# Kernel tuning notes

Hardware: AMD Instinct MI355X
Metric: run time of the kernel (lower is better)

Reference implementation:

```python
import jax, jax.numpy as jnp
import numpy as np

SPIKE_PROB = 0.3


def setup_inputs() -> dict:
    key = jax.random.key(0)
    T, B, C, H, W = 4, 32, 128, 56, 56
    u = jax.random.uniform(key, (T, B, C, H, W), dtype=jnp.float32)
    spikes = (u < SPIKE_PROB).astype(jnp.float32)  # binary spike trains
    return {"spikes": spikes, "TIME": T}


def reference(spikes, TIME):
    # spikes: [TIME, B, C, H, W] binary spike tensor, one slice per forward call.
    # Replicates Sparsity_Checker over a full TIME window:
    #   spike_collector accumulates spikes over t;
    #   sparsity_ratio = mean over t of per-step zero fraction (divided by TIME at t==TIME);
    #   temp_sparsity_ratio_of_collector = zero fraction of final collector;
    #   unique(return_counts) on integer-valued collector == bincount over 0..TIME.
    total = spikes[0].size  # elements per timestep

    # per-step zero fractions, then average over TIME (matches /= self.TIME)
    per_step_zero = jnp.sum(spikes == 0, axis=tuple(range(1, spikes.ndim)))  # [TIME]
    sparsity_ratio = jnp.sum(per_step_zero.astype(jnp.float32)) / (total * TIME)

    # final accumulated collector (state after the last forward call)
    collector = jnp.sum(spikes, axis=0)  # [B, C, H, W], integer-valued 0..TIME

    coll_zero_frac = jnp.sum(collector == 0).astype(jnp.float32) / total

    # histogram of collector values: unique_vals are 0..TIME, counts via bincount
    unique_counts = jnp.bincount(collector.astype(jnp.int32).ravel(), length=TIME + 1)

    # module returns the input spike unchanged; stats are side outputs
    return spikes, sparsity_ratio, coll_zero_frac, unique_counts
```

## Files before the change

### kernel.cpp

```cpp
#include <hip/hip_runtime.h>


constexpr int T_STEPS = 4;

__global__ __launch_bounds__(256) void spike_stats_kernel(
    const float4* __restrict__ in, float4* __restrict__ out,
    unsigned int* __restrict__ hist, int nvec)
{
    __shared__ unsigned int lhist[5];
    if (threadIdx.x < 5) lhist[threadIdx.x] = 0u;
    __syncthreads();

    unsigned long long packed = 0ull;

    const int stride = gridDim.x * blockDim.x;
    for (int v = blockIdx.x * blockDim.x + threadIdx.x; v < nvec; v += stride) {
        float4 a0 = in[0 * nvec + v];
        float4 a1 = in[1 * nvec + v];
        float4 a2 = in[2 * nvec + v];
        float4 a3 = in[3 * nvec + v];
        out[0 * nvec + v] = a0;
        out[1 * nvec + v] = a1;
        out[2 * nvec + v] = a2;
        out[3 * nvec + v] = a3;
        int cx = (int)(a0.x + a1.x + a2.x + a3.x);
        int cy = (int)(a0.y + a1.y + a2.y + a3.y);
        int cz = (int)(a0.z + a1.z + a2.z + a3.z);
        int cw = (int)(a0.w + a1.w + a2.w + a3.w);
        packed += (1ull << (cx * 12)) + (1ull << (cy * 12))
                + (1ull << (cz * 12)) + (1ull << (cw * 12));
    }

#pragma unroll
    for (int off = 32; off > 0; off >>= 1)
        packed += __shfl_down(packed, off, 64);

    if ((threadIdx.x & 63) == 0) {
#pragma unroll
        for (int k = 0; k < 5; ++k)
            atomicAdd(&lhist[k], (unsigned int)((packed >> (12 * k)) & 0xFFFull));
    }
    __syncthreads();

    if (threadIdx.x < 5)
        atomicAdd(&hist[threadIdx.x], lhist[threadIdx.x]);
}

__global__ void finalize_kernel(const unsigned int* __restrict__ hist,
                                float* __restrict__ tail, double total)
{
    if (threadIdx.x == 0 && blockIdx.x == 0) {
        double spikes_sum = 0.0;
#pragma unroll
        for (int k = 0; k < 5; ++k)
            spikes_sum += (double)k * (double)hist[k];
        double denom = total * (double)T_STEPS;
        tail[0] = (float)((denom - spikes_sum) / denom);
        tail[1] = (float)((double)hist[0] / total);
#pragma unroll
        for (int k = 0; k < 5; ++k)
            tail[2 + k] = (float)hist[k];
    }
}

extern "C" void kernel_launch(void* const* d_in, const int* in_sizes, int n_in,
                              void* d_out, int out_size, void* d_ws, size_t ws_size,
                              hipStream_t stream)
{
    const float* spikes = (const float*)d_in[0];
    float* out = (float*)d_out;

    const long n = (long)in_sizes[0];
    const long per_t = n / T_STEPS;
    const int nvec = (int)(per_t / 4);

    unsigned int* hist = (unsigned int*)d_ws;
    hipMemsetAsync(d_ws, 0, 5 * sizeof(unsigned int), stream);

    spike_stats_kernel<<<dim3(1024), dim3(256), 0, stream>>>(
        (const float4*)spikes, (float4*)out, hist, nvec);

    finalize_kernel<<<dim3(1), dim3(64), 0, stream>>>(hist, out + n, (double)per_t);
}
```

Before: 348.9 us.

## Fuse finalize into main kernel, use nontemporal loads/stores, double grid size

Switches global loads and stores to nontemporal builtins so the streamed copy does not pollute caches. It folds the separate finalize kernel into the stats kernel using a last-block-done counter, which removes one launch. It also doubles the grid from 1024 to 2048 blocks and vectorizes the four-way sum. The last-block pattern adds a threadfence and one more atomic per block.

New measurement: 443.6 us. 1.27x slower.

```diff
diff --git a/kernel.cpp b/kernel.cpp
--- a/kernel.cpp
+++ b/kernel.cpp
@@ -3,11 +3,15 @@
 
 constexpr int T_STEPS = 4;
 
+typedef float vfloat4 __attribute__((ext_vector_type(4)));
+
 __global__ __launch_bounds__(256) void spike_stats_kernel(
-    const float4* __restrict__ in, float4* __restrict__ out,
-    unsigned int* __restrict__ hist, int nvec)
+    const vfloat4* __restrict__ in, vfloat4* __restrict__ out,
+    unsigned int* __restrict__ hist,
+    float* __restrict__ tail, int nvec, double total)
 {
     __shared__ unsigned int lhist[5];
+    __shared__ unsigned int s_prev;
     if (threadIdx.x < 5) lhist[threadIdx.x] = 0u;
     __syncthreads();
 
@@ -15,20 +19,17 @@
 
     const int stride = gridDim.x * blockDim.x;
     for (int v = blockIdx.x * blockDim.x + threadIdx.x; v < nvec; v += stride) {
-        float4 a0 = in[0 * nvec + v];
-        float4 a1 = in[1 * nvec + v];
-        float4 a2 = in[2 * nvec + v];
-        float4 a3 = in[3 * nvec + v];
-        out[0 * nvec + v] = a0;
-        out[1 * nvec + v] = a1;
-        out[2 * nvec + v] = a2;
-        out[3 * nvec + v] = a3;
-        int cx = (int)(a0.x + a1.x + a2.x + a3.x);
-        int cy = (int)(a0.y + a1.y + a2.y + a3.y);
-        int cz = (int)(a0.z + a1.z + a2.z + a3.z);
-        int cw = (int)(a0.w + a1.w + a2.w + a3.w);
-        packed += (1ull << (cx * 12)) + (1ull << (cy * 12))
-                + (1ull << (cz * 12)) + (1ull << (cw * 12));
+        vfloat4 a0 = __builtin_nontemporal_load(&in[0 * nvec + v]);
+        vfloat4 a1 = __builtin_nontemporal_load(&in[1 * nvec + v]);
+        vfloat4 a2 = __builtin_nontemporal_load(&in[2 * nvec + v]);
+        vfloat4 a3 = __builtin_nontemporal_load(&in[3 * nvec + v]);
+        __builtin_nontemporal_store(a0, &out[0 * nvec + v]);
+        __builtin_nontemporal_store(a1, &out[1 * nvec + v]);
+        __builtin_nontemporal_store(a2, &out[2 * nvec + v]);
+        __builtin_nontemporal_store(a3, &out[3 * nvec + v]);
+        vfloat4 s = a0 + a1 + a2 + a3;
+        packed += (1ull << ((int)s.x * 12)) + (1ull << ((int)s.y * 12))
+                + (1ull << ((int)s.z * 12)) + (1ull << ((int)s.w * 12));
     }
 
 #pragma unroll
@@ -44,22 +45,28 @@
 
     if (threadIdx.x < 5)
         atomicAdd(&hist[threadIdx.x], lhist[threadIdx.x]);
-}
+    __syncthreads();
 
-__global__ void finalize_kernel(const unsigned int* __restrict__ hist,
-                                float* __restrict__ tail, double total)
-{
-    if (threadIdx.x == 0 && blockIdx.x == 0) {
+    if (threadIdx.x == 0) {
+        __threadfence();
+        s_prev = atomicAdd(&hist[5], 1u);
+    }
+    __syncthreads();
+    if (threadIdx.x == 0 && s_prev == gridDim.x - 1) {
+        unsigned int h[5];
+#pragma unroll
+        for (int k = 0; k < 5; ++k)
+            h[k] = atomicAdd(&hist[k], 0u);
         double spikes_sum = 0.0;
 #pragma unroll
         for (int k = 0; k < 5; ++k)
-            spikes_sum += (double)k * (double)hist[k];
+            spikes_sum += (double)k * (double)h[k];
         double denom = total * (double)T_STEPS;
         tail[0] = (float)((denom - spikes_sum) / denom);
-        tail[1] = (float)((double)hist[0] / total);
+        tail[1] = (float)((double)h[0] / total);
 #pragma unroll
         for (int k = 0; k < 5; ++k)
-            tail[2 + k] = (float)hist[k];
+            tail[2 + k] = (float)h[k];
     }
 }
 
@@ -75,10 +82,8 @@
     const int nvec = (int)(per_t / 4);
 
     unsigned int* hist = (unsigned int*)d_ws;
-    hipMemsetAsync(d_ws, 0, 5 * sizeof(unsigned int), stream);
+    (void)hipMemsetAsync(d_ws, 0, 6 * sizeof(unsigned int), stream);
 
-    spike_stats_kernel<<<dim3(1024), dim3(256), 0, stream>>>(
-        (const float4*)spikes, (float4*)out, hist, nvec);
-
-    finalize_kernel<<<dim3(1), dim3(64), 0, stream>>>(hist, out + n, (double)per_t);
+    spike_stats_kernel<<<dim3(2048), dim3(256), 0, stream>>>(
+        (const vfloat4*)spikes, (vfloat4*)out, hist, out + n, nvec, (double)per_t);
 }
```
